# Kernel optimization log

Hardware: AMD Instinct MI355X
Metric: run time of the kernel (lower is better)

The kernel has to match this reference:

```python
import jax, jax.numpy as jnp
import numpy as np

H, W = 480, 640
B = 4
P = 10          # number of accumulated flow passes (num_flows = 1)
N = 400000      # events per batch element
TREF = 1.0
TS_SCALING = 1.0
SPAT_W = 1.0
TEMP_W = 1.0


def _corners(loc):
    """loc: [M,2] (y,x) float -> flattened corner idx [4M] int32, bilinear weights [4M].
    Corner order: TL, TR, BL, BR (blocks of M), matching pol_mask repeat(1,4,1) layout.
    Out-of-grid corners get zero weight; indices are clamped in-range."""
    ty = jnp.floor(loc[:, 0:1])
    lx = jnp.floor(loc[:, 1:2])
    cs = jnp.concatenate([
        jnp.concatenate([ty, lx], 1),
        jnp.concatenate([ty, lx + 1.0], 1),
        jnp.concatenate([ty + 1.0, lx], 1),
        jnp.concatenate([ty + 1.0, lx + 1.0], 1)], axis=0)  # [4M,2]
    w = jnp.maximum(0.0, 1.0 - jnp.abs(jnp.tile(loc, (4, 1)) - cs))
    weights = w[:, 0] * w[:, 1]
    inb = ((cs[:, 0] >= 0) & (cs[:, 0] <= H - 1) &
           (cs[:, 1] >= 0) & (cs[:, 1] <= W - 1))
    weights = weights * inb.astype(weights.dtype)
    idx = (jnp.clip(cs[:, 0], 0, H - 1) * W + jnp.clip(cs[:, 1], 0, W - 1)).astype(jnp.int32)
    return idx, weights


def setup_inputs() -> dict:
    key = jax.random.key(0)
    k1, k2, k3, k4, k5 = jax.random.split(key, 5)
    scale = jnp.array([H - 1.0, W - 1.0], dtype=jnp.float32)
    warped_events = jax.random.uniform(k1, (B, N, 2), dtype=jnp.float32) * scale
    pos = jax.random.bernoulli(k2, 0.5, (B, N)).astype(jnp.float32)
    pos4 = jnp.tile(pos, (1, 4))                                   # [B,4N]
    pol_mask = jnp.stack([pos4, 1.0 - pos4], axis=-1)              # [B,4N,2]
    ts = jax.random.uniform(k3, (B, N, 1), dtype=jnp.float32)
    ts_list = jnp.tile(ts, (1, 4, 1))                              # [B,4N,1]
    flow_x = jax.random.normal(k4, (B, P, H, W), dtype=jnp.float32) * 3.0
    flow_y = jax.random.normal(k5, (B, P, H, W), dtype=jnp.float32) * 3.0
    return {"warped_events": warped_events, "pol_mask": pol_mask,
            "ts_list": ts_list, "flow_x": flow_x, "flow_y": flow_y}


def reference(warped_events, pol_mask, ts_list, flow_x, flow_y):
    f32 = flow_x.dtype
    # ---- iwe_formatting: bilinear scatter-add of warped events ----
    idx, weights = jax.vmap(_corners)(warped_events)               # [B,4N], [B,4N]
    norm_ts = 1.0 - jnp.abs(TREF - ts_list[..., 0]) / TS_SCALING   # [B,4N]

    def scat(i, w):
        return jnp.zeros(H * W, w.dtype).at[i].add(w)

    def img(w):
        return jax.vmap(scat)(idx, w).reshape(B, 1, H, W)

    iwe = jnp.concatenate([img(weights * pol_mask[:, :, 0]),
                           img(weights * pol_mask[:, :, 1])], axis=1)          # [B,2,H,W]
    iwe_ts = jnp.concatenate([img(weights * norm_ts * pol_mask[:, :, 0]),
                              img(weights * norm_ts * pol_mask[:, :, 1])], axis=1)

    # ---- focus_loss ----
    ts2 = iwe_ts.reshape(B, 2, -1)
    fl = jnp.sum(ts2[:, 0] ** 2, axis=1) + jnp.sum(ts2[:, 1] ** 2, axis=1)
    nz = (jnp.sum(iwe, axis=1) != 0).reshape(B, -1)
    fl = fl / (jnp.sum(nz, axis=1) + 1e-9)
    focus = jnp.sum(fl)

    # ---- flow_temporal_smoothing: warp grid by flow[j], gather flow[j+1] ----
    grid = jnp.stack(jnp.meshgrid(jnp.arange(H, dtype=f32),
                                  jnp.arange(W, dtype=f32), indexing='ij'), 0)  # [2,H,W] (y,x)
    flow = jnp.stack([flow_y[:, :-1], flow_x[:, :-1]], axis=2)                  # [B,P-1,2,H,W]
    loc = (grid[None, None] + flow).reshape(B, P - 1, 2, H * W).transpose(0, 1, 3, 2)  # [B,P-1,HW,2]
    m = ((loc[..., 0] >= 0) & (loc[..., 0] <= H - 1) &
         (loc[..., 1] >= 0) & (loc[..., 1] <= W - 1)).astype(f32)

    def samp(fx, fy, l):
        # fx, fy: [H,W]; l: [HW,2] -> sampled (y,x) flow [HW,2]
        i, w = _corners(l)
        sx = (fx.reshape(-1)[i] * w).reshape(4, -1).sum(0)
        sy = (fy.reshape(-1)[i] * w).reshape(4, -1).sum(0)
        return jnp.stack([sy, sx], axis=-1)

    wf = jax.vmap(jax.vmap(samp))(flow_x[:, 1:], flow_y[:, 1:], loc)            # [B,P-1,HW,2]
    ff = flow.reshape(B, P - 1, 2, H * W).transpose(0, 1, 3, 2)
    dt = jnp.sum(jnp.sqrt((ff - wf) ** 2 + 1e-9), axis=-1)                      # [B,P-1,HW]
    lt = jnp.sum(dt * m, axis=-1) / (jnp.sum(m, axis=-1) + 1e-9)                # [B,P-1]
    temporal = TEMP_W * jnp.sum(jnp.sum(lt, axis=1) / (P - 1))                  # num_flows = 1

    # ---- flow_spatial_smoothing: Charbonnier on 4 neighbor directions ----
    def charb(a):
        return jnp.sqrt(a ** 2 + 1e-6)

    dx = charb(flow_x[..., :-1] - flow_x[..., 1:]) + charb(flow_y[..., :-1] - flow_y[..., 1:])
    dy = charb(flow_x[:, :, :-1, :] - flow_x[:, :, 1:, :]) + charb(flow_y[:, :, :-1, :] - flow_y[:, :, 1:, :])
    ddr = charb(flow_x[:, :, :-1, :-1] - flow_x[:, :, 1:, 1:]) + charb(flow_y[:, :, :-1, :-1] - flow_y[:, :, 1:, 1:])
    dur = charb(flow_x[:, :, 1:, :-1] - flow_x[:, :, :-1, 1:]) + charb(flow_y[:, :, 1:, :-1] - flow_y[:, :, :-1, 1:])
    mm = lambda t: t.reshape(B, P, -1).mean(2).mean(1)
    spatial = SPAT_W * jnp.sum((mm(dx) + mm(dy) + mm(ddr) + mm(dur)) / 4.0)

    return focus + temporal + spatial
```

## Files before the change

### kernel.cpp

```cpp
#include <hip/hip_runtime.h>

#define BB 4
#define PP 10
#define NN 400000
#define HH 480
#define WW 640
constexpr int HW    = HH * WW;
constexpr int NXB   = HW / 256;
constexpr int NXB4  = HW / 1024;
constexpr int NTILE = NXB4 * BB * PP;
constexpr int CHUNK = NTILE / 8;
constexpr int EVB   = (BB * NN + NTILE - 1) / NTILE;

constexpr int QW = WW / 2, QH = HH / 2, QN = QW * QH;
constexpr size_t IMG_QUADS = (size_t)4 * BB * 2 * QN;

constexpr float SCALE     = 1024.0f;
constexpr float INV_SCALE = 1.0f / 1024.0f;

constexpr int PF_V = 0;
constexpr int PF_N = PF_V + BB * NXB;
constexpr int PT_D = PF_N + BB * NXB;
constexpr int PT_M = PT_D + BB * (PP-1) * NXB4 * 4;
constexpr int PS   = PT_M + BB * (PP-1) * NXB4 * 4;
constexpr int NPART = PS + BB * PP * NXB4 * 4;


__device__ __forceinline__ float fsq(float a) { return __builtin_amdgcn_sqrtf(a); }
__device__ __forceinline__ float charb(float a) { return fsq(fmaf(a, a, 1e-6f)); }

__device__ __forceinline__ void waveSum3(float& a, float& b, float& c) {
    #pragma unroll
    for (int off = 32; off > 0; off >>= 1) {
        a += __shfl_down(a, off, 64);
        b += __shfl_down(b, off, 64);
        c += __shfl_down(c, off, 64);
    }
}

__device__ __forceinline__ float blockSum256(float v, float* smem) {
    #pragma unroll
    for (int off = 32; off > 0; off >>= 1)
        v += __shfl_down(v, off, 64);
    int lane = threadIdx.x & 63;
    int wid  = threadIdx.x >> 6;
    if (lane == 0) smem[wid] = v;
    __syncthreads();
    float r = 0.f;
    if (threadIdx.x == 0) r = smem[0] + smem[1] + smem[2] + smem[3];
    __syncthreads();
    return r;
}

__device__ __forceinline__ void scatter_one(int e,
                                            const float2* __restrict__ we,
                                            const float* __restrict__ pol,
                                            const float* __restrict__ tsl,
                                            unsigned long long* __restrict__ img) {
    int b = e / NN;
    int m = e - b * NN;
    float2 c = we[e];
    float y = c.x, x = c.y;
    float pm0 = pol[((size_t)b * 4 * NN + m) * 2];
    float ts  = tsl[(size_t)b * 4 * NN + m];
    float nts = 1.0f - fabsf(1.0f - ts);
    float tyf = fminf(fmaxf(floorf(y), 0.f), (float)(HH - 2));
    float lxf = fminf(fmaxf(floorf(x), 0.f), (float)(WW - 2));
    float fy_ = y - tyf, fx_ = x - lxf;
    float gy = 1.f - fy_, gx = 1.f - fx_;
    float s = nts * SCALE;
    unsigned long long wTL = (unsigned int)(gy * gx * s + 0.5f);
    unsigned long long wTR = (unsigned int)(gy * fx_ * s + 0.5f);
    unsigned long long wBL = (unsigned int)(fy_ * gx * s + 0.5f);
    unsigned long long wBR = (unsigned int)(fy_ * fx_ * s + 0.5f);
    unsigned long long val = wTL | (wTR << 16) | (wBL << 32) | (wBR << 48);
    int ty = (int)tyf, lx = (int)lxf;
    int pi = ((ty & 1) << 1) | (lx & 1);
    int pl = (pm0 > 0.5f) ? 0 : 1;
    size_t wi = ((size_t)((pi * BB + b) * 2 + pl)) * QN + (ty >> 1) * QW + (lx >> 1);
    atomicAdd(&img[wi], val);
}


__global__ __launch_bounds__(256)
void fused_kernel(const float2* __restrict__ we,
                  const float* __restrict__ pol,
                  const float* __restrict__ tsl,
                  const float* __restrict__ FX, const float* __restrict__ FY,
                  unsigned long long* __restrict__ img,
                  float* __restrict__ part) {
    int w = blockIdx.x;
    int t = threadIdx.x;

    int l  = (w & 7) * CHUNK + (w >> 3);
    int bp = l / NXB4;
    int xb = l - bp * NXB4;
    int b2 = bp / PP;
    int j  = bp - b2 * PP;
    const float* fx = FX + (size_t)bp * HW;
    const float* fy = FY + (size_t)bp * HW;

    int p0 = xb * 1024 + t * 4;
    int y  = p0 / WW;
    int x0 = p0 - y * WW;
    float4 vx = *(const float4*)(fx + p0);
    float4 vy = *(const float4*)(fy + p0);
    bool yin  = (y + 1 < HH);
    bool xend = (x0 == WW - 4);
    float4 bx4 = make_float4(0.f, 0.f, 0.f, 0.f), by4 = bx4;
    float vxr = 0.f, vyr = 0.f, bxr = 0.f, byr = 0.f;
    if (yin) {
        bx4 = *(const float4*)(fx + p0 + WW);
        by4 = *(const float4*)(fy + p0 + WW);
    }
    if (!xend) { vxr = fx[p0 + 4]; vyr = fy[p0 + 4]; }
    if (yin && !xend) { bxr = fx[p0 + WW + 4]; byr = fy[p0 + WW + 4]; }

    constexpr float cdx = 1.0f / ((float)HH * (WW - 1) * 4.0f * PP);
    constexpr float cdy = 1.0f / ((float)(HH - 1) * WW * 4.0f * PP);
    constexpr float cdd = 1.0f / ((float)(HH - 1) * (WW - 1) * 4.0f * PP);

    float acc = 0.f;
    acc += (charb(vx.x - vx.y) + charb(vy.x - vy.y)) * cdx;
    acc += (charb(vx.y - vx.z) + charb(vy.y - vy.z)) * cdx;
    acc += (charb(vx.z - vx.w) + charb(vy.z - vy.w)) * cdx;
    if (!xend) acc += (charb(vx.w - vxr) + charb(vy.w - vyr)) * cdx;
    if (yin) {
        acc += (charb(vx.x - bx4.x) + charb(vy.x - by4.x)) * cdy;
        acc += (charb(vx.y - bx4.y) + charb(vy.y - by4.y)) * cdy;
        acc += (charb(vx.z - bx4.z) + charb(vy.z - by4.z)) * cdy;
        acc += (charb(vx.w - bx4.w) + charb(vy.w - by4.w)) * cdy;
        acc += (charb(vx.x - bx4.y) + charb(vy.x - by4.y)) * cdd;
        acc += (charb(vx.y - bx4.z) + charb(vy.y - by4.z)) * cdd;
        acc += (charb(vx.z - bx4.w) + charb(vy.z - by4.w)) * cdd;
        acc += (charb(bx4.x - vx.y) + charb(by4.x - vy.y)) * cdd;
        acc += (charb(bx4.y - vx.z) + charb(by4.y - vy.z)) * cdd;
        acc += (charb(bx4.z - vx.w) + charb(by4.z - vy.w)) * cdd;
        if (!xend) {
            acc += (charb(vx.w - bxr) + charb(vy.w - byr)) * cdd;
            acc += (charb(bx4.w - vxr) + charb(by4.w - vyr)) * cdd;
        }
    }

    float td = 0.f, tm = 0.f;
    if (j < PP - 1) {
        const float* gx1 = fx + HW;
        const float* gy1 = fy + HW;
        #pragma unroll
        for (int k = 0; k < 4; ++k) {
            int p  = xb * 1024 + k * 256 + t;
            int yy = p / WW;
            int xx = p - yy * WW;
            float fx00 = fx[p];
            float fy00 = fy[p];
            float ly  = (float)yy + fy00;
            float lx2 = (float)xx + fx00;
            bool m = (ly >= 0.f) && (ly <= (float)(HH - 1)) &&
                     (lx2 >= 0.f) && (lx2 <= (float)(WW - 1));
            if (m) {
                tm += 1.f;
                float tyf = fminf(fmaxf(floorf(ly),  0.f), (float)(HH - 2));
                float txf = fminf(fmaxf(floorf(lx2), 0.f), (float)(WW - 2));
                float fyy = ly - tyf, fxx = lx2 - txf;
                float gyy = 1.f - fyy, gxx = 1.f - fxx;
                int pix = (int)tyf * WW + (int)txf;
                float sx = gyy * (gxx * gx1[pix]      + fxx * gx1[pix + 1]) +
                           fyy * (gxx * gx1[pix + WW] + fxx * gx1[pix + WW + 1]);
                float sy = gyy * (gxx * gy1[pix]      + fxx * gy1[pix + 1]) +
                           fyy * (gxx * gy1[pix + WW] + fxx * gy1[pix + WW + 1]);
                float dy_ = fy00 - sy;
                float dx_ = fx00 - sx;
                td += fsq(fmaf(dy_, dy_, 1e-9f)) + fsq(fmaf(dx_, dx_, 1e-9f));
            }
        }
    }

    __builtin_amdgcn_sched_barrier(0);
    int e = w * EVB + t;
    if (t < EVB && e < BB * NN)
        scatter_one(e, we, pol, tsl, img);
    __builtin_amdgcn_sched_barrier(0);

    waveSum3(acc, td, tm);
    if ((t & 63) == 0) {
        int wid = t >> 6;
        part[PS + (bp * NXB4 + xb) * 4 + wid] = acc;
        if (j < PP - 1) {
            int bj = b2 * (PP - 1) + j;
            part[PT_D + (bj * NXB4 + xb) * 4 + wid] = td;
            part[PT_M + (bj * NXB4 + xb) * 4 + wid] = tm;
        }
    }
}


__global__ __launch_bounds__(256)
void focus_kernel(const unsigned long long* __restrict__ img,
                  float* __restrict__ part) {
    __shared__ float sm[8];
    int b = blockIdx.y;
    int p = blockIdx.x * 256 + threadIdx.x;
    int y = p / WW;
    int x = p - y * WW;
    unsigned int sp = 0, sn = 0;
    #pragma unroll
    for (int dy = 0; dy < 2; ++dy) {
        #pragma unroll
        for (int dx = 0; dx < 2; ++dx) {
            int ty = y - dy, lx = x - dx;
            if (ty < 0 || lx < 0 || ty > HH - 2 || lx > WW - 2) continue;
            int pi = ((ty & 1) << 1) | (lx & 1);
            size_t base = ((size_t)(pi * BB + b) * 2) * QN + (ty >> 1) * QW + (lx >> 1);
            int sh = 16 * ((dy << 1) | dx);
            sp += (unsigned int)((img[base]      >> sh) & 0xFFFFull);
            sn += (unsigned int)((img[base + QN] >> sh) & 0xFFFFull);
        }
    }
    float tp = (float)sp * INV_SCALE;
    float tn = (float)sn * INV_SCALE;
    float v  = tp * tp + tn * tn;
    float nz = ((sp | sn) != 0u) ? 1.f : 0.f;
    float sv  = blockSum256(v, sm);
    float snz = blockSum256(nz, sm + 4);
    if (threadIdx.x == 0) {
        part[PF_V + b * NXB + blockIdx.x] = sv;
        part[PF_N + b * NXB + blockIdx.x] = snz;
    }
}


__global__ __launch_bounds__(256)
void reduce_kernel(const float* __restrict__ part, float* __restrict__ seg) {
    __shared__ float sm[4];
    int s = blockIdx.x;
    int base, len;
    if (s < 4)       { base = PF_V + s * NXB;             len = NXB; }
    else if (s < 8)  { base = PF_N + (s - 4) * NXB;       len = NXB; }
    else if (s < 44) { base = PT_D + (s - 8) * NXB4 * 4;  len = NXB4 * 4; }
    else if (s < 80) { base = PT_M + (s - 44) * NXB4 * 4; len = NXB4 * 4; }
    else             { base = PS;                         len = BB * PP * NXB4 * 4; }
    float v = 0.f;
    for (int i = threadIdx.x; i < len; i += 256) v += part[base + i];
    float r = blockSum256(v, sm);
    if (threadIdx.x == 0) seg[s] = r;
}


__global__ void final_kernel(const float* __restrict__ seg, float* __restrict__ out) {
    if (threadIdx.x == 0 && blockIdx.x == 0) {
        float focus = 0.f;
        #pragma unroll
        for (int b = 0; b < BB; ++b)
            focus += seg[b] / (seg[BB + b] + 1e-9f);
        float temporal = 0.f;
        #pragma unroll
        for (int k = 0; k < BB * (PP - 1); ++k)
            temporal += seg[8 + k] / (seg[44 + k] + 1e-9f);
        temporal *= 1.0f / (float)(PP - 1);
        out[0] = focus + temporal + seg[80];
    }
}


extern "C" void kernel_launch(void* const* d_in, const int* in_sizes, int n_in,
                              void* d_out, int out_size, void* d_ws, size_t ws_size,
                              hipStream_t stream) {
    const float2* we  = (const float2*)d_in[0];
    const float*  pol = (const float*)d_in[1];
    const float*  tsl = (const float*)d_in[2];
    const float*  FX  = (const float*)d_in[3];
    const float*  FY  = (const float*)d_in[4];
    float*              seg  = (float*)d_ws;
    unsigned long long* img  = (unsigned long long*)(seg + 256);
    float*              part = (float*)(img + IMG_QUADS);

    hipMemsetAsync(img, 0, IMG_QUADS * sizeof(unsigned long long), stream);

    fused_kernel<<<NTILE, 256, 0, stream>>>(we, pol, tsl, FX, FY, img, part);
    focus_kernel<<<dim3(NXB, BB), 256, 0, stream>>>(img, part);
    reduce_kernel<<<81, 256, 0, stream>>>(part, seg);
    final_kernel<<<1, 64, 0, stream>>>(seg, (float*)d_out);
}
```

Baseline: 182.0 us.

## Tile fused kernel in 2D and stage next-flow window in LDS for warps

Each fused block now handles a 64x16 2D tile of one flow field instead of a 1024-pixel linear strip. For the temporal term, it first loads a 41x89 halo window of the next pass's flow into shared memory, so the bilinear warp samples come from LDS and fall back to global memory only outside the window. The temporal term now reuses the already-loaded float4 flow values instead of reloading them. This trades extra halo loads, an LDS staging pass and a barrier for fewer scattered global gathers. The larger LDS footprint may lower occupancy.

```diff
diff --git a/kernel.cpp b/kernel.cpp
--- a/kernel.cpp
+++ b/kernel.cpp
@@ -7,10 +7,13 @@
 #define WW 640
 constexpr int HW    = HH * WW;
 constexpr int NXB   = HW / 256;
-constexpr int NXB4  = HW / 1024;
-constexpr int NTILE = NXB4 * BB * PP;
+constexpr int TLW   = 64, TLH = 16;
+constexpr int NXT   = (WW / TLW) * (HH / TLH);
+constexpr int NTILE = NXT * BB * PP;
 constexpr int CHUNK = NTILE / 8;
 constexpr int EVB   = (BB * NN + NTILE - 1) / NTILE;
+
+constexpr int WR = 41, WC = 89, WCP = 90;
 
 constexpr int QW = WW / 2, QH = HH / 2, QN = QW * QH;
 constexpr size_t IMG_QUADS = (size_t)4 * BB * 2 * QN;
@@ -21,9 +24,9 @@
 constexpr int PF_V = 0;
 constexpr int PF_N = PF_V + BB * NXB;
 constexpr int PT_D = PF_N + BB * NXB;
-constexpr int PT_M = PT_D + BB * (PP-1) * NXB4 * 4;
-constexpr int PS   = PT_M + BB * (PP-1) * NXB4 * 4;
-constexpr int NPART = PS + BB * PP * NXB4 * 4;
+constexpr int PT_M = PT_D + BB * (PP-1) * NXT * 4;
+constexpr int PS   = PT_M + BB * (PP-1) * NXT * 4;
+constexpr int NPART = PS + BB * PP * NXT * 4;
 
 
 __device__ __forceinline__ float fsq(float a) { return __builtin_amdgcn_sqrtf(a); }
@@ -89,24 +92,42 @@
                   const float* __restrict__ FX, const float* __restrict__ FY,
                   unsigned long long* __restrict__ img,
                   float* __restrict__ part) {
+    __shared__ float sfx[WR][WCP];
+    __shared__ float sfy[WR][WCP];
     int w = blockIdx.x;
     int t = threadIdx.x;
 
     int l  = (w & 7) * CHUNK + (w >> 3);
-    int bp = l / NXB4;
-    int xb = l - bp * NXB4;
+    int bp = l / NXT;
+    int xb = l - bp * NXT;
     int b2 = bp / PP;
     int j  = bp - b2 * PP;
+    int x0 = (xb % (WW / TLW)) * TLW;
+    int y0 = (xb / (WW / TLW)) * TLH;
     const float* fx = FX + (size_t)bp * HW;
     const float* fy = FY + (size_t)bp * HW;
-
-    int p0 = xb * 1024 + t * 4;
-    int y  = p0 / WW;
-    int x0 = p0 - y * WW;
+    const float* gx1 = fx + HW;
+    const float* gy1 = fy + HW;
+    bool hasT = (j < PP - 1);
+
+    int wy0 = y0 - 12, wx0 = x0 - 12;
+    if (hasT) {
+        for (int idx = t; idx < WR * WC; idx += 256) {
+            int r = idx / WC, c = idx - r * WC;
+            int gy = min(max(wy0 + r, 0), HH - 1);
+            int gc = min(max(wx0 + c, 0), WW - 1);
+            sfx[r][c] = gx1[gy * WW + gc];
+            sfy[r][c] = gy1[gy * WW + gc];
+        }
+    }
+
+    int ypx = y0 + (t >> 4);
+    int xpx = x0 + (t & 15) * 4;
+    int p0  = ypx * WW + xpx;
     float4 vx = *(const float4*)(fx + p0);
     float4 vy = *(const float4*)(fy + p0);
-    bool yin  = (y + 1 < HH);
-    bool xend = (x0 == WW - 4);
+    bool yin  = (ypx + 1 < HH);
+    bool xend = (xpx == WW - 4);
     float4 bx4 = make_float4(0.f, 0.f, 0.f, 0.f), by4 = bx4;
     float vxr = 0.f, vyr = 0.f, bxr = 0.f, byr = 0.f;
     if (yin) {
@@ -143,33 +164,42 @@
     }
 
     float td = 0.f, tm = 0.f;
-    if (j < PP - 1) {
-        const float* gx1 = fx + HW;
-        const float* gy1 = fy + HW;
+    if (hasT) {
+        __syncthreads();
+        float ax[4] = {vx.x, vx.y, vx.z, vx.w};
+        float ay[4] = {vy.x, vy.y, vy.z, vy.w};
         #pragma unroll
-        for (int k = 0; k < 4; ++k) {
-            int p  = xb * 1024 + k * 256 + t;
-            int yy = p / WW;
-            int xx = p - yy * WW;
-            float fx00 = fx[p];
-            float fy00 = fy[p];
-            float ly  = (float)yy + fy00;
-            float lx2 = (float)xx + fx00;
+        for (int i = 0; i < 4; ++i) {
+            float ly  = (float)ypx + ay[i];
+            float lx2 = (float)(xpx + i) + ax[i];
             bool m = (ly >= 0.f) && (ly <= (float)(HH - 1)) &&
                      (lx2 >= 0.f) && (lx2 <= (float)(WW - 1));
             if (m) {
                 tm += 1.f;
                 float tyf = fminf(fmaxf(floorf(ly),  0.f), (float)(HH - 2));
                 float txf = fminf(fmaxf(floorf(lx2), 0.f), (float)(WW - 2));
+                int ity = (int)tyf, itx = (int)txf;
                 float fyy = ly - tyf, fxx = lx2 - txf;
                 float gyy = 1.f - fyy, gxx = 1.f - fxx;
-                int pix = (int)tyf * WW + (int)txf;
-                float sx = gyy * (gxx * gx1[pix]      + fxx * gx1[pix + 1]) +
-                           fyy * (gxx * gx1[pix + WW] + fxx * gx1[pix + WW + 1]);
-                float sy = gyy * (gxx * gy1[pix]      + fxx * gy1[pix + 1]) +
-                           fyy * (gxx * gy1[pix + WW] + fxx * gy1[pix + WW + 1]);
-                float dy_ = fy00 - sy;
-                float dx_ = fx00 - sx;
+                float x00, x01, x10, x11, y00, y01, y10, y11;
+                if (ity >= wy0 && ity <= wy0 + WR - 2 &&
+                    itx >= wx0 && itx <= wx0 + WC - 2) {
+                    int r = ity - wy0, c = itx - wx0;
+                    x00 = sfx[r][c];     x01 = sfx[r][c + 1];
+                    x10 = sfx[r + 1][c]; x11 = sfx[r + 1][c + 1];
+                    y00 = sfy[r][c];     y01 = sfy[r][c + 1];
+                    y10 = sfy[r + 1][c]; y11 = sfy[r + 1][c + 1];
+                } else {
+                    int pix = ity * WW + itx;
+                    x00 = gx1[pix];      x01 = gx1[pix + 1];
+                    x10 = gx1[pix + WW]; x11 = gx1[pix + WW + 1];
+                    y00 = gy1[pix];      y01 = gy1[pix + 1];
+                    y10 = gy1[pix + WW]; y11 = gy1[pix + WW + 1];
+                }
+                float sx = gyy * (gxx * x00 + fxx * x01) + fyy * (gxx * x10 + fxx * x11);
+                float sy = gyy * (gxx * y00 + fxx * y01) + fyy * (gxx * y10 + fxx * y11);
+                float dy_ = ay[i] - sy;
+                float dx_ = ax[i] - sx;
                 td += fsq(fmaf(dy_, dy_, 1e-9f)) + fsq(fmaf(dx_, dx_, 1e-9f));
             }
         }
@@ -184,11 +214,11 @@
     waveSum3(acc, td, tm);
     if ((t & 63) == 0) {
         int wid = t >> 6;
-        part[PS + (bp * NXB4 + xb) * 4 + wid] = acc;
-        if (j < PP - 1) {
+        part[PS + (bp * NXT + xb) * 4 + wid] = acc;
+        if (hasT) {
             int bj = b2 * (PP - 1) + j;
-            part[PT_D + (bj * NXB4 + xb) * 4 + wid] = td;
-            part[PT_M + (bj * NXB4 + xb) * 4 + wid] = tm;
+            part[PT_D + (bj * NXT + xb) * 4 + wid] = td;
+            part[PT_M + (bj * NXT + xb) * 4 + wid] = tm;
         }
     }
 }
@@ -234,11 +264,11 @@
     __shared__ float sm[4];
     int s = blockIdx.x;
     int base, len;
-    if (s < 4)       { base = PF_V + s * NXB;             len = NXB; }
-    else if (s < 8)  { base = PF_N + (s - 4) * NXB;       len = NXB; }
-    else if (s < 44) { base = PT_D + (s - 8) * NXB4 * 4;  len = NXB4 * 4; }
-    else if (s < 80) { base = PT_M + (s - 44) * NXB4 * 4; len = NXB4 * 4; }
-    else             { base = PS;                         len = BB * PP * NXB4 * 4; }
+    if (s < 4)       { base = PF_V + s * NXB;            len = NXB; }
+    else if (s < 8)  { base = PF_N + (s - 4) * NXB;      len = NXB; }
+    else if (s < 44) { base = PT_D + (s - 8) * NXT * 4;  len = NXT * 4; }
+    else if (s < 80) { base = PT_M + (s - 44) * NXT * 4; len = NXT * 4; }
+    else             { base = PS;                        len = BB * PP * NXT * 4; }
     float v = 0.f;
     for (int i = threadIdx.x; i < len; i += 256) v += part[base + i];
     float r = blockSum256(v, sm);
```

Result: no change. 180.3 us (-0.9%).
